# Optimization experiments

Measured on AMD Instinct MI355X. Metric: run time of the kernel, lower is better.

The kernel has to match this reference:

```python
import jax, jax.numpy as jnp
import numpy as np

B, CIN, COUT, MODES, RES = 64, 64, 64, 16, 8192


def setup_inputs() -> dict:
    key = jax.random.key(0)
    kx, kr, ki = jax.random.split(key, 3)
    scale = 1.0 / (CIN * COUT)
    x = jax.random.normal(kx, (B, CIN, RES), dtype=jnp.float32)
    w_real = jax.random.normal(kr, (CIN, COUT, MODES), dtype=jnp.float32) * scale
    w_imag = jax.random.normal(ki, (CIN, COUT, MODES), dtype=jnp.float32) * scale
    return {"x": x, "w_real": w_real, "w_imag": w_imag}


def reference(x, w_real, w_imag):
    # x: [B, Cin, N] real; weight: [Cin, Cout, modes] complex
    batch, _, n = x.shape
    modes = w_real.shape[-1]
    cout = w_real.shape[1]
    w = w_real + 1j * w_imag
    x_ft = jnp.fft.rfft(x)                      # [B, Cin, N//2+1] complex64
    # single batched complex contraction over all kept modes
    out_modes = jnp.einsum('bim,iom->bom', x_ft[:, :, :modes], w)  # [B, Cout, modes]
    out_ft = jnp.zeros((batch, cout, x_ft.shape[-1]), dtype=out_modes.dtype)
    out_ft = out_ft.at[:, :, :modes].set(out_modes)
    return jnp.fft.irfft(out_ft, n=n)           # [B, Cout, N] real
```

## Files before the change

kernel.cpp:

```cpp
#include <hip/hip_runtime.h>
#include <math.h>


#define B_     64
#define CIN_   64
#define COUT_  64
#define MODES_ 16
#define RES_   8192
#define NA     512
#define PITCH  522

__device__ static constexpr float COS16[16] = {
     1.0f,  0.92387953251128674f,  0.70710678118654752f,  0.38268343236508977f,
     0.0f, -0.38268343236508977f, -0.70710678118654752f, -0.92387953251128674f,
    -1.0f, -0.92387953251128674f, -0.70710678118654752f, -0.38268343236508977f,
     0.0f,  0.38268343236508977f,  0.70710678118654752f,  0.92387953251128674f
};
__device__ static constexpr float SIN16[16] = {
     0.0f,  0.38268343236508977f,  0.70710678118654752f,  0.92387953251128674f,
     1.0f,  0.92387953251128674f,  0.70710678118654752f,  0.38268343236508977f,
     0.0f, -0.38268343236508977f, -0.70710678118654752f, -0.92387953251128674f,
    -1.0f, -0.92387953251128674f, -0.70710678118654752f, -0.38268343236508977f
};

#define W8192 7.66990393942820428e-4f

__global__ __launch_bounds__(256) void kA(const float* __restrict__ x,
                                          float* __restrict__ X) {
    __shared__ float Ts[18 * PITCH];
    __shared__ float P[16][17][2];
    const int row = blockIdx.x;
    const int tid = threadIdx.x;
    const float* __restrict__ xr = x + (size_t)row * RES_;

    float2 m[16];
#pragma unroll
    for (int b = 0; b < 16; ++b)
        m[b] = *(const float2*)(xr + 2 * tid + NA * b);

    float2 x0 = m[0], x8 = m[8];
    float2 ev[8], ov[8];
#pragma unroll
    for (int b = 1; b <= 7; ++b) {
        ev[b].x = m[b].x + m[16 - b].x;  ev[b].y = m[b].y + m[16 - b].y;
        ov[b].x = m[b].x - m[16 - b].x;  ov[b].y = m[b].y - m[16 - b].y;
    }
#pragma unroll
    for (int k = 0; k <= 8; ++k) {
        float sr0 = (k & 1) ? (x0.x - x8.x) : (x0.x + x8.x);
        float sr1 = (k & 1) ? (x0.y - x8.y) : (x0.y + x8.y);
        float si0 = 0.f, si1 = 0.f;
#pragma unroll
        for (int b = 1; b <= 7; ++b) {
            const float cc = COS16[(k * b) & 15];
            const float ss = SIN16[(k * b) & 15];
            sr0 = fmaf(ev[b].x, cc, sr0);
            sr1 = fmaf(ev[b].y, cc, sr1);
            si0 = fmaf(ov[b].x, -ss, si0);
            si1 = fmaf(ov[b].y, -ss, si1);
        }
        *(float2*)&Ts[(2 * k) * PITCH + 2 * tid]     = make_float2(sr0, sr1);
        *(float2*)&Ts[(2 * k + 1) * PITCH + 2 * tid] = make_float2(si0, si1);
    }
    __syncthreads();

    const int k  = tid & 15;
    const int c  = tid >> 4;
    const int kp = (k <= 8) ? k : 16 - k;
    const float sgn = (k <= 8) ? 1.f : -1.f;
    float sA, cA, sB, cB;
    __sincosf((float)(k * c)  * W8192, &sA, &cA);
    __sincosf((float)(k * 16) * W8192, &sB, &cB);
    float wre = cA, wim = -sA;
    const float sre = cB, sim = -sB;
    float accr = 0.f, acci = 0.f;
    const float* __restrict__ Tr = &Ts[(2 * kp) * PITCH + c];
    const float* __restrict__ Ti = &Ts[(2 * kp + 1) * PITCH + c];
#pragma unroll 8
    for (int j = 0; j < 32; ++j) {
        const float tr = Tr[16 * j];
        const float ti = sgn * Ti[16 * j];
        accr = fmaf(wre, tr, fmaf(-wim, ti, accr));
        acci = fmaf(wre, ti, fmaf( wim, tr, acci));
        const float nre = fmaf(wre, sre, -wim * sim);
        wim = fmaf(wre, sim, wim * sre);
        wre = nre;
    }
    P[k][c][0] = accr;
    P[k][c][1] = acci;
    __syncthreads();
    if (tid < 16) {
        float xre = 0.f, xim = 0.f;
#pragma unroll
        for (int c2 = 0; c2 < 16; ++c2) { xre += P[tid][c2][0]; xim += P[tid][c2][1]; }
        *(float2*)&X[row * 32 + 2 * tid] = make_float2(xre, xim);
    }
}

__global__ __launch_bounds__(256) void kC(const float* __restrict__ X,
                                          const float* __restrict__ wr,
                                          const float* __restrict__ wi,
                                          float* __restrict__ y) {
    __shared__ float Xs[CIN_ * 32];
    __shared__ float Ps[16][17][2];
    __shared__ float Csh[32];
    const int row = blockIdx.x;
    const int b = row >> 6, o = row & 63;
    const int tid = threadIdx.x;

    const float4* __restrict__ Xb4 = (const float4*)(X + (size_t)b * CIN_ * 32);
    for (int t = tid; t < CIN_ * 8; t += 256)
        ((float4*)Xs)[t] = Xb4[t];
    __syncthreads();

    {
        const int k = tid & 15, p = tid >> 4;
        float pr = 0.f, pi = 0.f;
#pragma unroll
        for (int mI = 0; mI < 4; ++mI) {
            const int i = 4 * p + mI;
            const float xre = Xs[i * 32 + 2 * k];
            const float xim = Xs[i * 32 + 2 * k + 1];
            const float wrv = wr[(i * COUT_ + o) * MODES_ + k];
            const float wiv = wi[(i * COUT_ + o) * MODES_ + k];
            pr = fmaf(xre, wrv, fmaf(-xim, wiv, pr));
            pi = fmaf(xre, wiv, fmaf( xim, wrv, pi));
        }
        Ps[k][p][0] = pr;
        Ps[k][p][1] = pi;
    }
    __syncthreads();
    if (tid < 32) {
        const int k = tid & 15, comp = tid >> 4;
        float s = 0.f;
#pragma unroll
        for (int p = 0; p < 16; ++p) s += Ps[k][p][comp];
        const float g = (k == 0) ? (1.0f / RES_) : (2.0f / RES_);
        Csh[2 * k + comp] = g * s;
    }
    __syncthreads();

    float C[32];
#pragma unroll
    for (int q = 0; q < 8; ++q) {
        const float4 v = ((const float4*)Csh)[q];
        C[4 * q] = v.x; C[4 * q + 1] = v.y; C[4 * q + 2] = v.z; C[4 * q + 3] = v.w;
    }

    float* __restrict__ yr = y + (size_t)row * RES_;
    float yv[16][2];
#pragma unroll
    for (int half = 0; half < 2; ++half) {
        const int a = 2 * tid + half;
        float su, cu;
        __sincosf((float)a * W8192, &su, &cu);
        float wre = 1.f, wim = 0.f;
        float Er0 = 0.f, Er8 = 0.f, Er[8], Oi[8];
#pragma unroll
        for (int q = 1; q <= 7; ++q) { Er[q] = 0.f; Oi[q] = 0.f; }
#pragma unroll
        for (int k = 0; k < 16; ++k) {
            const float cre = C[2 * k], cim = C[2 * k + 1];
            const float dre = fmaf(cre, wre, -cim * wim);
            const float dim = fmaf(cre, wim,  cim * wre);
            if (k == 0)      { Er0 = dre; }
            else if (k == 8) { Er8 = dre; }
            else if (k < 8)  { Er[k]      += dre; Oi[k]      += dim; }
            else             { Er[16 - k] += dre; Oi[16 - k] -= dim; }
            const float nre = fmaf(wre, cu, -wim * su);
            wim = fmaf(wre, su, wim * cu);
            wre = nre;
        }
#pragma unroll
        for (int bb = 0; bb <= 8; ++bb) {
            float Cc = (bb & 1) ? (Er0 - Er8) : (Er0 + Er8);
            float Ss = 0.f;
#pragma unroll
            for (int q = 1; q <= 7; ++q) {
                Cc = fmaf(Er[q], COS16[(q * bb) & 15], Cc);
                Ss = fmaf(Oi[q], SIN16[(q * bb) & 15], Ss);
            }
            if (bb == 0)      yv[0][half] = Cc;
            else if (bb == 8) yv[8][half] = Cc;
            else { yv[bb][half] = Cc - Ss; yv[16 - bb][half] = Cc + Ss; }
        }
    }
#pragma unroll
    for (int bb = 0; bb < 16; ++bb)
        *(float2*)(yr + NA * bb + 2 * tid) = make_float2(yv[bb][0], yv[bb][1]);
}

extern "C" void kernel_launch(void* const* d_in, const int* in_sizes, int n_in,
                              void* d_out, int out_size, void* d_ws, size_t ws_size,
                              hipStream_t stream) {
    const float* x  = (const float*)d_in[0];
    const float* wr = (const float*)d_in[1];
    const float* wi = (const float*)d_in[2];
    float* out = (float*)d_out;
    float* X = (float*)d_ws;

    kA<<<dim3(B_ * CIN_), dim3(256), 0, stream>>>(x, X);
    kC<<<dim3(B_ * COUT_), dim3(256), 0, stream>>>(X, wr, wi, out);
}
```

Baseline: 238.1 us.

## Double threads per block, one element per thread, wave-shuffle reductions

Both kernels now launch 512 threads per row, and each thread handles one column of the 16x512 decomposition instead of two. The shared twiddle table is packed as float2 with an odd pitch, and the partial mode sums are reduced with cross-lane shuffles instead of a full shared-memory reduction. The synthesis kernel broadcasts the coefficients into scalar registers via readfirstlane. The aim is more parallelism, lower register pressure per thread and cheaper reductions, at the cost of scalar per-thread loads and stores that are less wide.

```diff
diff --git a/kernel.cpp b/kernel.cpp
--- a/kernel.cpp
+++ b/kernel.cpp
@@ -8,7 +8,8 @@
 #define MODES_ 16
 #define RES_   8192
 #define NA     512
-#define PITCH  522
+#define TPITCH 515
+#define W8192  7.66990393942820428e-4f
 
 __device__ static constexpr float COS16[16] = {
      1.0f,  0.92387953251128674f,  0.70710678118654752f,  0.38268343236508977f,
@@ -23,44 +24,31 @@
     -1.0f, -0.92387953251128674f, -0.70710678118654752f, -0.38268343236508977f
 };
 
-#define W8192 7.66990393942820428e-4f
-
-__global__ __launch_bounds__(256) void kA(const float* __restrict__ x,
-                                          float* __restrict__ X) {
-    __shared__ float Ts[18 * PITCH];
-    __shared__ float P[16][17][2];
+__global__ __launch_bounds__(512, 8) void kA(const float* __restrict__ x,
+                                             float* __restrict__ X) {
+    __shared__ float2 Ts[9 * TPITCH];
+    __shared__ float  Pred[8][16][2];
     const int row = blockIdx.x;
     const int tid = threadIdx.x;
     const float* __restrict__ xr = x + (size_t)row * RES_;
 
-    float2 m[16];
-#pragma unroll
-    for (int b = 0; b < 16; ++b)
-        m[b] = *(const float2*)(xr + 2 * tid + NA * b);
-
-    float2 x0 = m[0], x8 = m[8];
-    float2 ev[8], ov[8];
-#pragma unroll
-    for (int b = 1; b <= 7; ++b) {
-        ev[b].x = m[b].x + m[16 - b].x;  ev[b].y = m[b].y + m[16 - b].y;
-        ov[b].x = m[b].x - m[16 - b].x;  ov[b].y = m[b].y - m[16 - b].y;
-    }
+    float m[16];
+#pragma unroll
+    for (int b = 0; b < 16; ++b) m[b] = xr[tid + NA * b];
+    float ev[8], ov[8];
+#pragma unroll
+    for (int b = 1; b <= 7; ++b) { ev[b] = m[b] + m[16 - b]; ov[b] = m[b] - m[16 - b]; }
+    const float x0 = m[0], x8 = m[8];
 #pragma unroll
     for (int k = 0; k <= 8; ++k) {
-        float sr0 = (k & 1) ? (x0.x - x8.x) : (x0.x + x8.x);
-        float sr1 = (k & 1) ? (x0.y - x8.y) : (x0.y + x8.y);
-        float si0 = 0.f, si1 = 0.f;
+        float sr = (k & 1) ? (x0 - x8) : (x0 + x8);
+        float si = 0.f;
 #pragma unroll
         for (int b = 1; b <= 7; ++b) {
-            const float cc = COS16[(k * b) & 15];
-            const float ss = SIN16[(k * b) & 15];
-            sr0 = fmaf(ev[b].x, cc, sr0);
-            sr1 = fmaf(ev[b].y, cc, sr1);
-            si0 = fmaf(ov[b].x, -ss, si0);
-            si1 = fmaf(ov[b].y, -ss, si1);
-        }
-        *(float2*)&Ts[(2 * k) * PITCH + 2 * tid]     = make_float2(sr0, sr1);
-        *(float2*)&Ts[(2 * k + 1) * PITCH + 2 * tid] = make_float2(si0, si1);
+            sr = fmaf(ev[b],  COS16[(k * b) & 15], sr);
+            si = fmaf(ov[b], -SIN16[(k * b) & 15], si);
+        }
+        Ts[k * TPITCH + tid] = make_float2(sr, si);
     }
     __syncthreads();
 
@@ -70,55 +58,56 @@
     const float sgn = (k <= 8) ? 1.f : -1.f;
     float sA, cA, sB, cB;
     __sincosf((float)(k * c)  * W8192, &sA, &cA);
-    __sincosf((float)(k * 16) * W8192, &sB, &cB);
-    float wre = cA, wim = -sA;
-    const float sre = cB, sim = -sB;
+    __sincosf((float)(k * 32) * W8192, &sB, &cB);
+    float wre = cA, wim = -sgn * sA;
+    const float sre = cB, sim = -sgn * sB;
     float accr = 0.f, acci = 0.f;
-    const float* __restrict__ Tr = &Ts[(2 * kp) * PITCH + c];
-    const float* __restrict__ Ti = &Ts[(2 * kp + 1) * PITCH + c];
-#pragma unroll 8
-    for (int j = 0; j < 32; ++j) {
-        const float tr = Tr[16 * j];
-        const float ti = sgn * Ti[16 * j];
-        accr = fmaf(wre, tr, fmaf(-wim, ti, accr));
-        acci = fmaf(wre, ti, fmaf( wim, tr, acci));
+    const float2* __restrict__ Tp = &Ts[kp * TPITCH + c];
+#pragma unroll
+    for (int j = 0; j < 16; ++j) {
+        const float2 t = Tp[32 * j];
+        accr = fmaf(wre, t.x, fmaf(-wim, t.y, accr));
+        acci = fmaf(wre, t.y, fmaf( wim, t.x, acci));
         const float nre = fmaf(wre, sre, -wim * sim);
         wim = fmaf(wre, sim, wim * sre);
         wre = nre;
     }
-    P[k][c][0] = accr;
-    P[k][c][1] = acci;
-    __syncthreads();
-    if (tid < 16) {
-        float xre = 0.f, xim = 0.f;
-#pragma unroll
-        for (int c2 = 0; c2 < 16; ++c2) { xre += P[tid][c2][0]; xim += P[tid][c2][1]; }
-        *(float2*)&X[row * 32 + 2 * tid] = make_float2(xre, xim);
+    acci *= sgn;
+    accr += __shfl_xor(accr, 16, 64);  acci += __shfl_xor(acci, 16, 64);
+    accr += __shfl_xor(accr, 32, 64);  acci += __shfl_xor(acci, 32, 64);
+    if ((tid & 63) < 16) {
+        *(float2*)&Pred[tid >> 6][k][0] = make_float2(accr, acci);
+    }
+    __syncthreads();
+    if (tid < 32) {
+        const int kk = tid >> 1, comp = tid & 1;
+        float s = 0.f;
+#pragma unroll
+        for (int w = 0; w < 8; ++w) s += Pred[w][kk][comp];
+        X[row * 32 + tid] = s;
     }
 }
 
-__global__ __launch_bounds__(256) void kC(const float* __restrict__ X,
-                                          const float* __restrict__ wr,
-                                          const float* __restrict__ wi,
-                                          float* __restrict__ y) {
+__global__ __launch_bounds__(512, 8) void kC(const float* __restrict__ X,
+                                             const float* __restrict__ wr,
+                                             const float* __restrict__ wi,
+                                             float* __restrict__ y) {
     __shared__ float Xs[CIN_ * 32];
-    __shared__ float Ps[16][17][2];
+    __shared__ float Pred[8][16][2];
     __shared__ float Csh[32];
     const int row = blockIdx.x;
     const int b = row >> 6, o = row & 63;
     const int tid = threadIdx.x;
 
-    const float4* __restrict__ Xb4 = (const float4*)(X + (size_t)b * CIN_ * 32);
-    for (int t = tid; t < CIN_ * 8; t += 256)
-        ((float4*)Xs)[t] = Xb4[t];
+    ((float4*)Xs)[tid] = ((const float4*)(X + (size_t)b * CIN_ * 32))[tid];
     __syncthreads();
 
     {
         const int k = tid & 15, p = tid >> 4;
         float pr = 0.f, pi = 0.f;
 #pragma unroll
-        for (int mI = 0; mI < 4; ++mI) {
-            const int i = 4 * p + mI;
+        for (int mI = 0; mI < 2; ++mI) {
+            const int i = 2 * p + mI;
             const float xre = Xs[i * 32 + 2 * k];
             const float xim = Xs[i * 32 + 2 * k + 1];
             const float wrv = wr[(i * COUT_ + o) * MODES_ + k];
@@ -126,68 +115,86 @@
             pr = fmaf(xre, wrv, fmaf(-xim, wiv, pr));
             pi = fmaf(xre, wiv, fmaf( xim, wrv, pi));
         }
-        Ps[k][p][0] = pr;
-        Ps[k][p][1] = pi;
+        pr += __shfl_xor(pr, 16, 64);  pi += __shfl_xor(pi, 16, 64);
+        pr += __shfl_xor(pr, 32, 64);  pi += __shfl_xor(pi, 32, 64);
+        if ((tid & 63) < 16) *(float2*)&Pred[tid >> 6][k][0] = make_float2(pr, pi);
     }
     __syncthreads();
     if (tid < 32) {
-        const int k = tid & 15, comp = tid >> 4;
+        const int kk = tid >> 1, comp = tid & 1;
         float s = 0.f;
 #pragma unroll
-        for (int p = 0; p < 16; ++p) s += Ps[k][p][comp];
-        const float g = (k == 0) ? (1.0f / RES_) : (2.0f / RES_);
-        Csh[2 * k + comp] = g * s;
-    }
-    __syncthreads();
-
-    float C[32];
-#pragma unroll
-    for (int q = 0; q < 8; ++q) {
-        const float4 v = ((const float4*)Csh)[q];
-        C[4 * q] = v.x; C[4 * q + 1] = v.y; C[4 * q + 2] = v.z; C[4 * q + 3] = v.w;
-    }
-
-    float* __restrict__ yr = y + (size_t)row * RES_;
-    float yv[16][2];
-#pragma unroll
-    for (int half = 0; half < 2; ++half) {
-        const int a = 2 * tid + half;
-        float su, cu;
-        __sincosf((float)a * W8192, &su, &cu);
-        float wre = 1.f, wim = 0.f;
-        float Er0 = 0.f, Er8 = 0.f, Er[8], Oi[8];
-#pragma unroll
-        for (int q = 1; q <= 7; ++q) { Er[q] = 0.f; Oi[q] = 0.f; }
-#pragma unroll
-        for (int k = 0; k < 16; ++k) {
-            const float cre = C[2 * k], cim = C[2 * k + 1];
-            const float dre = fmaf(cre, wre, -cim * wim);
-            const float dim = fmaf(cre, wim,  cim * wre);
-            if (k == 0)      { Er0 = dre; }
-            else if (k == 8) { Er8 = dre; }
-            else if (k < 8)  { Er[k]      += dre; Oi[k]      += dim; }
-            else             { Er[16 - k] += dre; Oi[16 - k] -= dim; }
+        for (int w = 0; w < 8; ++w) s += Pred[w][kk][comp];
+        const float g = (kk == 0) ? (1.0f / RES_) : (2.0f / RES_);
+        Csh[tid] = g * s;
+    }
+    __syncthreads();
+
+    float cr[16], ci[16];
+#pragma unroll
+    for (int kk = 0; kk < 16; ++kk) {
+        cr[kk] = __int_as_float(__builtin_amdgcn_readfirstlane(__float_as_int(Csh[2 * kk])));
+        ci[kk] = __int_as_float(__builtin_amdgcn_readfirstlane(__float_as_int(Csh[2 * kk + 1])));
+    }
+
+    float su, cu;
+    __sincosf((float)tid * W8192, &su, &cu);
+    float wre = cu, wim = su;
+    float Er0 = cr[0];
+    float Er[8], Oi[8], Er8;
+#pragma unroll
+    for (int k = 1; k <= 7; ++k) {
+        Er[k] = fmaf(cr[k], wre, -ci[k] * wim);
+        Oi[k] = fmaf(cr[k], wim,  ci[k] * wre);
+        const float nre = fmaf(wre, cu, -wim * su);
+        wim = fmaf(wre, su, wim * cu);
+        wre = nre;
+    }
+    Er8 = fmaf(cr[8], wre, -ci[8] * wim);
+    {
+        const float nre = fmaf(wre, cu, -wim * su);
+        wim = fmaf(wre, su, wim * cu);
+        wre = nre;
+    }
+#pragma unroll
+    for (int k = 9; k <= 15; ++k) {
+        const int q = 16 - k;
+        Er[q] = fmaf( cr[k], wre, Er[q]);
+        Er[q] = fmaf(-ci[k], wim, Er[q]);
+        Oi[q] = fmaf(-cr[k], wim, Oi[q]);
+        Oi[q] = fmaf(-ci[k], wre, Oi[q]);
+        if (k < 15) {
             const float nre = fmaf(wre, cu, -wim * su);
             wim = fmaf(wre, su, wim * cu);
             wre = nre;
         }
-#pragma unroll
-        for (int bb = 0; bb <= 8; ++bb) {
-            float Cc = (bb & 1) ? (Er0 - Er8) : (Er0 + Er8);
-            float Ss = 0.f;
-#pragma unroll
-            for (int q = 1; q <= 7; ++q) {
-                Cc = fmaf(Er[q], COS16[(q * bb) & 15], Cc);
-                Ss = fmaf(Oi[q], SIN16[(q * bb) & 15], Ss);
-            }
-            if (bb == 0)      yv[0][half] = Cc;
-            else if (bb == 8) yv[8][half] = Cc;
-            else { yv[bb][half] = Cc - Ss; yv[16 - bb][half] = Cc + Ss; }
-        }
-    }
-#pragma unroll
-    for (int bb = 0; bb < 16; ++bb)
-        *(float2*)(yr + NA * bb + 2 * tid) = make_float2(yv[bb][0], yv[bb][1]);
+    }
+
+    float* __restrict__ yr = y + (size_t)row * RES_ + tid;
+    {
+        float Cc = Er0 + Er8;
+#pragma unroll
+        for (int q = 1; q <= 7; ++q) Cc += Er[q];
+        yr[0] = Cc;
+    }
+    {
+        float Cc = Er0 + Er8;
+#pragma unroll
+        for (int q = 1; q <= 7; ++q) Cc += (q & 1) ? -Er[q] : Er[q];
+        yr[NA * 8] = Cc;
+    }
+#pragma unroll
+    for (int bb = 1; bb <= 7; ++bb) {
+        float Cc = (bb & 1) ? (Er0 - Er8) : (Er0 + Er8);
+        float Ss = 0.f;
+#pragma unroll
+        for (int q = 1; q <= 7; ++q) {
+            Cc = fmaf(Er[q], COS16[(q * bb) & 15], Cc);
+            Ss = fmaf(Oi[q], SIN16[(q * bb) & 15], Ss);
+        }
+        yr[NA * bb]        = Cc - Ss;
+        yr[NA * (16 - bb)] = Cc + Ss;
+    }
 }
 
 extern "C" void kernel_launch(void* const* d_in, const int* in_sizes, int n_in,
@@ -199,6 +206,6 @@
     float* out = (float*)d_out;
     float* X = (float*)d_ws;
 
-    kA<<<dim3(B_ * CIN_), dim3(256), 0, stream>>>(x, X);
-    kC<<<dim3(B_ * COUT_), dim3(256), 0, stream>>>(X, wr, wi, out);
+    kA<<<dim3(B_ * CIN_), dim3(512), 0, stream>>>(x, X);
+    kC<<<dim3(B_ * COUT_), dim3(512), 0, stream>>>(X, wr, wi, out);
 }
```

Result: no change. 236.6 us (-0.6%).
